# Kernel optimization log

Measured on AMD Instinct MI355X. Metric: run time of the kernel, lower is better.

## Reference

```python
import jax, jax.numpy as jnp
import numpy as np

B, D, H, A, P = 262144, 256, 4, 32, 4
GAMMA = 2.0
SCALE = A ** -0.5
EPS = 1e-5


def _ln(x, g, b):
    m = jnp.mean(x, axis=-1, keepdims=True)
    v = jnp.mean((x - m) ** 2, axis=-1, keepdims=True)
    return (x - m) * jax.lax.rsqrt(v + EPS) * g + b


def setup_inputs() -> dict:
    key = jax.random.key(0)
    ks = jax.random.split(key, 16)
    r = D // 4  # ClassConditionalGate reduction
    return {
        "x": jax.random.normal(ks[0], (B, D), jnp.float32),
        "minority_prob": jax.random.uniform(ks[1], (B, 1), jnp.float32),
        "Wq": jax.random.normal(ks[2], (H, D, A), jnp.float32) * (D ** -0.5),
        "bq": jnp.zeros((H, A), jnp.float32),
        "proto_keys": jax.random.normal(ks[3], (H, P, A), jnp.float32) * 0.02,
        "proto_values": jax.random.normal(ks[4], (H, P, A), jnp.float32) * 0.02,
        "proto_importance": jnp.full((H, P), 1.0 / P, jnp.float32),
        "focal_alpha": jnp.array([0.6 * (1 + 0.1 * i) for i in range(H)], jnp.float32),
        "focal_temp": jnp.ones((H,), jnp.float32),
        "Wo": jax.random.normal(ks[5], (H, A, A), jnp.float32) * (A ** -0.5),
        "bo": jnp.zeros((H, A), jnp.float32),
        "ln_g": jnp.ones((H, A), jnp.float32),
        "ln_b": jnp.zeros((H, A), jnp.float32),
        "Wf": jax.random.normal(ks[6], (H * A, D), jnp.float32) * ((H * A) ** -0.5),
        "bf": jnp.zeros((D,), jnp.float32),
        "Wg1": jax.random.normal(ks[7], (D + 1, r), jnp.float32) * ((D + 1) ** -0.5),
        "bg1": jnp.zeros((r,), jnp.float32),
        "Wg2": jax.random.normal(ks[8], (r, D), jnp.float32) * (r ** -0.5),
        "bg2": jnp.zeros((D,), jnp.float32),
        "lnF_g": jnp.ones((D,), jnp.float32),
        "lnF_b": jnp.zeros((D,), jnp.float32),
    }


def reference(x, minority_prob, Wq, bq, proto_keys, proto_values, proto_importance,
              focal_alpha, focal_temp, Wo, bo, ln_g, ln_b, Wf, bf,
              Wg1, bg1, Wg2, bg2, lnF_g, lnF_b):
    # all heads batched over leading H axis (dropout is identity in eval)
    q = jnp.einsum("bd,hda->bha", x, Wq) + bq                       # [B,H,A]
    scores = jnp.einsum("bha,hpa->bhp", q, proto_keys) + proto_importance
    # focal modulation: uncertainty per sample, per-head alpha/temp
    uncertainty = 1.0 - jnp.abs(minority_prob - 0.5) * 2.0           # [B,1]
    fw = focal_alpha * (uncertainty + 1e-8) ** GAMMA * focal_temp    # [B,H]
    scores = scores * (1.0 + fw[:, :, None])
    w = jax.nn.softmax(scores * SCALE, axis=-1)                      # [B,H,P]
    attended = jnp.einsum("bhp,hpa->bha", w, proto_values)
    h_out = jnp.einsum("bha,hao->bho", attended, Wo) + bo
    h_out = _ln(h_out, ln_g, ln_b)                                   # per-head LN
    combined = h_out.reshape(h_out.shape[0], H * A)                  # cat over heads
    out = combined @ Wf + bf                                         # [B,D]
    # class-conditional gate
    difficulty = 1.0 - 2.0 * jnp.abs(minority_prob - 0.5)            # [B,1]
    gi = jnp.concatenate([out, difficulty], axis=-1)
    gate = jax.nn.sigmoid(jax.nn.relu(gi @ Wg1 + bg1) @ Wg2 + bg2)
    out = out * gate
    return _ln(out + x, lnF_g, lnF_b)
```

## Files before the change

kernel.cpp:

```cpp
#include <hip/hip_runtime.h>
#include <math.h>

typedef __bf16 bf16;
typedef __bf16 bf16x8 __attribute__((ext_vector_type(8)));
typedef float f32x4 __attribute__((ext_vector_type(4)));

#define MFMA16(a,b,c) __builtin_amdgcn_mfma_f32_16x16x32_bf16((a),(b),(c),0,0,0)

#define D 256
#define H 4
#define A 32
#define P 4
#define HA 128
#define RHID 64
#define ROWS 64
#define NROWS_TOT 262144
#define SQP 136
#define SCALE_F 0.17677669529663687f

#define OFF_Q  0
#define OFF_F  32768
#define OFF_G1 65536
#define OFF_G2 81920
#define OFF_O  98304
#define NPACK  102400

__global__ __launch_bounds__(256)
void prep_kernel(const float* __restrict__ Wq, const float* __restrict__ Wf,
                 const float* __restrict__ Wg1, const float* __restrict__ Wg2,
                 const float* __restrict__ Wo, bf16* __restrict__ ws)
{
  int i = blockIdx.x * 256 + threadIdx.x;
  if (i >= NPACK) return;
  float v;
  if (i < OFF_F) {
    int j = i & 7, l = (i >> 3) & 63, nt = (i >> 9) & 1, ks = (i >> 10) & 7, h = i >> 13;
    int k = ks * 32 + (l >> 4) * 8 + j, n = nt * 16 + (l & 15);
    v = Wq[(h * 256 + k) * 32 + n];
  } else if (i < OFF_G1) {
    int ii = i - OFF_F;
    int j = ii & 7, l = (ii >> 3) & 63, g = (ii >> 9) & 15, ks = ii >> 13;
    int k = ks * 32 + (l >> 4) * 8 + j, n = g * 16 + (l & 15);
    v = Wf[k * 256 + n];
  } else if (i < OFF_G2) {
    int ii = i - OFF_G1;
    int j = ii & 7, l = (ii >> 3) & 63, nt = (ii >> 9) & 3, ks = ii >> 11;
    int k = ks * 32 + (l >> 4) * 8 + j, n = nt * 16 + (l & 15);
    v = Wg1[k * 64 + n];
  } else if (i < OFF_O) {
    int ii = i - OFF_G2;
    int j = ii & 7, l = (ii >> 3) & 63, g = (ii >> 9) & 15, ks = ii >> 13;
    int k = ks * 32 + (l >> 4) * 8 + j, n = g * 16 + (l & 15);
    v = Wg2[k * 256 + n];
  } else {
    int ii = i - OFF_O;
    int j = ii & 7, l = (ii >> 3) & 63, nt = (ii >> 9) & 1, h = ii >> 10;
    int k = (l >> 4) * 8 + j, n = nt * 16 + (l & 15);
    v = Wo[(h * 32 + k) * 32 + n];
  }
  ws[i] = (bf16)v;
}

__global__ __launch_bounds__(256, 2)
void faiia_kernel(const float* __restrict__ x, const float* __restrict__ mp,
    const float* __restrict__ bq, const float* __restrict__ pk,
    const float* __restrict__ pv, const float* __restrict__ imp,
    const float* __restrict__ fa, const float* __restrict__ ft,
    const float* __restrict__ bo, const float* __restrict__ lng,
    const float* __restrict__ lnb, const float* __restrict__ bfb,
    const float* __restrict__ Wg1, const float* __restrict__ bg1,
    const float* __restrict__ bg2, const float* __restrict__ lnFg,
    const float* __restrict__ lnFb, const bf16* __restrict__ ws,
    float* __restrict__ out)
{
  __shared__ __attribute__((aligned(16))) bf16 s_regA[16384];
  __shared__ __attribute__((aligned(16))) bf16 s_q[ROWS * SQP];
  __shared__ __attribute__((aligned(16))) bf16 s_hfrag[4096];
  __shared__ float s_pk[H*P*A], s_pv[H*P*A], s_imp[H*P], s_fa[H], s_ft[H];
  __shared__ float s_bq[HA], s_bo[HA], s_lng[HA], s_lnb[HA];
  __shared__ float s_bf[D], s_bg1[RHID], s_wg1d[RHID], s_bg2[D], s_lnFg[D], s_lnFb[D];
  __shared__ float s_diff[ROWS];
  __shared__ float s_lnsum[ROWS*4], s_lnsq[ROWS*4], s_rmean[ROWS], s_rrstd[ROWS];

  const int t = threadIdx.x;
  const int lane = t & 63;
  const int w = t >> 6;
  const int lr = lane >> 4;
  const int lc = lane & 15;
  const int row0 = blockIdx.x * ROWS;

  for (int i = t; i < H*P*A; i += 256) { s_pk[i] = pk[i]; s_pv[i] = pv[i]; }
  if (t < H*P) s_imp[t] = imp[t];
  if (t < H) { s_fa[t] = fa[t]; s_ft[t] = ft[t]; }
  if (t < HA) { s_bq[t] = bq[t]; s_bo[t] = bo[t]; s_lng[t] = lng[t]; s_lnb[t] = lnb[t]; }
  s_bf[t] = bfb[t]; s_bg2[t] = bg2[t]; s_lnFg[t] = lnFg[t]; s_lnFb[t] = lnFb[t];
  if (t < RHID) { s_bg1[t] = bg1[t]; s_wg1d[t] = Wg1[256*RHID + t]; }
  if (t < ROWS) { float m = mp[row0 + t]; s_diff[t] = 1.f - 2.f*fabsf(m - 0.5f); }

  {
    const float* xbase = x + (size_t)row0 * D;
    #pragma unroll
    for (int i = 0; i < 8; ++i) {
      int s = t + 256*i;
      int l = s & 63, ks = (s >> 6) & 7, mt = s >> 9;
      int row = mt*16 + (l & 15);
      int k0 = ks*32 + ((l >> 4) & 3)*8;
      const float* xp = xbase + row*D + k0;
      float4 v0 = *reinterpret_cast<const float4*>(xp);
      float4 v1 = *reinterpret_cast<const float4*>(xp + 4);
      bf16x8 fr;
      fr[0]=(bf16)v0.x; fr[1]=(bf16)v0.y; fr[2]=(bf16)v0.z; fr[3]=(bf16)v0.w;
      fr[4]=(bf16)v1.x; fr[5]=(bf16)v1.y; fr[6]=(bf16)v1.z; fr[7]=(bf16)v1.w;
      *reinterpret_cast<bf16x8*>(&s_regA[(size_t)s * 8]) = fr;
    }
  }
  __syncthreads();

  {
    f32x4 acc[4][2];
    #pragma unroll
    for (int mt = 0; mt < 4; ++mt) { acc[mt][0] = (f32x4)0.f; acc[mt][1] = (f32x4)0.f; }
    const bf16x8* pQ = reinterpret_cast<const bf16x8*>(ws + OFF_Q);
    #pragma unroll
    for (int ks = 0; ks < 8; ++ks) {
      bf16x8 b0 = pQ[((w*8 + ks)*2 + 0)*64 + lane];
      bf16x8 b1 = pQ[((w*8 + ks)*2 + 1)*64 + lane];
      #pragma unroll
      for (int mt = 0; mt < 4; ++mt) {
        bf16x8 a = *reinterpret_cast<const bf16x8*>(&s_regA[((mt*8 + ks)*64 + lane)*8]);
        acc[mt][0] = MFMA16(a, b0, acc[mt][0]);
        acc[mt][1] = MFMA16(a, b1, acc[mt][1]);
      }
    }
    float bq0 = s_bq[w*32 + lc], bq1 = s_bq[w*32 + 16 + lc];
    #pragma unroll
    for (int mt = 0; mt < 4; ++mt)
      #pragma unroll
      for (int r = 0; r < 4; ++r) {
        int row = mt*16 + lr*4 + r;
        s_q[row*SQP + w*32 + lc]      = (bf16)(acc[mt][0][r] + bq0);
        s_q[row*SQP + w*32 + 16 + lc] = (bf16)(acc[mt][1][r] + bq1);
      }
  }
  __syncthreads();

  {
    const int r = t >> 2, h = t & 3;
    float q[32];
    #pragma unroll
    for (int g = 0; g < 4; ++g) {
      bf16x8 v = *reinterpret_cast<const bf16x8*>(&s_q[r*SQP + h*32 + g*8]);
      #pragma unroll
      for (int j = 0; j < 8; ++j) q[g*8 + j] = (float)v[j];
    }
    float u = s_diff[r];
    float up = u + 1e-8f;
    float mod = 1.f + s_fa[h]*up*up*s_ft[h];
    float sc[4];
    #pragma unroll
    for (int p = 0; p < 4; ++p) {
      float s = s_imp[h*4 + p];
      const float4* kp = reinterpret_cast<const float4*>(&s_pk[(h*4 + p)*32]);
      #pragma unroll
      for (int g = 0; g < 8; ++g) {
        float4 kv = kp[g];
        s = fmaf(q[g*4+0], kv.x, s); s = fmaf(q[g*4+1], kv.y, s);
        s = fmaf(q[g*4+2], kv.z, s); s = fmaf(q[g*4+3], kv.w, s);
      }
      sc[p] = s * mod * SCALE_F;
    }
    float mx = fmaxf(fmaxf(sc[0], sc[1]), fmaxf(sc[2], sc[3]));
    float e0 = expf(sc[0]-mx), e1 = expf(sc[1]-mx), e2 = expf(sc[2]-mx), e3 = expf(sc[3]-mx);
    float inv = 1.f / (e0+e1+e2+e3);
    e0 *= inv; e1 *= inv; e2 *= inv; e3 *= inv;
    const float4* p0 = reinterpret_cast<const float4*>(&s_pv[(h*4+0)*32]);
    const float4* p1 = reinterpret_cast<const float4*>(&s_pv[(h*4+1)*32]);
    const float4* p2 = reinterpret_cast<const float4*>(&s_pv[(h*4+2)*32]);
    const float4* p3 = reinterpret_cast<const float4*>(&s_pv[(h*4+3)*32]);
    const int mt = r >> 4, rl = r & 15;
    #pragma unroll
    for (int g = 0; g < 4; ++g) {
      float4 a0 = p0[g*2],   b0v = p0[g*2+1];
      float4 a1 = p1[g*2],   b1v = p1[g*2+1];
      float4 a2 = p2[g*2],   b2v = p2[g*2+1];
      float4 a3 = p3[g*2],   b3v = p3[g*2+1];
      bf16x8 av;
      av[0] = (bf16)(e0*a0.x + e1*a1.x + e2*a2.x + e3*a3.x);
      av[1] = (bf16)(e0*a0.y + e1*a1.y + e2*a2.y + e3*a3.y);
      av[2] = (bf16)(e0*a0.z + e1*a1.z + e2*a2.z + e3*a3.z);
      av[3] = (bf16)(e0*a0.w + e1*a1.w + e2*a2.w + e3*a3.w);
      av[4] = (bf16)(e0*b0v.x + e1*b1v.x + e2*b2v.x + e3*b3v.x);
      av[5] = (bf16)(e0*b0v.y + e1*b1v.y + e2*b2v.y + e3*b3v.y);
      av[6] = (bf16)(e0*b0v.z + e1*b1v.z + e2*b2v.z + e3*b3v.z);
      av[7] = (bf16)(e0*b0v.w + e1*b1v.w + e2*b2v.w + e3*b3v.w);
      *reinterpret_cast<bf16x8*>(&s_regA[(((h*4) + mt)*64 + g*16 + rl)*8]) = av;
    }
  }
  __syncthreads();

  {
    f32x4 acc[4][2];
    #pragma unroll
    for (int mt = 0; mt < 4; ++mt) { acc[mt][0] = (f32x4)0.f; acc[mt][1] = (f32x4)0.f; }
    const bf16x8* pO = reinterpret_cast<const bf16x8*>(ws + OFF_O);
    bf16x8 b0 = pO[(w*2 + 0)*64 + lane];
    bf16x8 b1 = pO[(w*2 + 1)*64 + lane];
    #pragma unroll
    for (int mt = 0; mt < 4; ++mt) {
      bf16x8 a = *reinterpret_cast<const bf16x8*>(&s_regA[((w*4 + mt)*64 + lane)*8]);
      acc[mt][0] = MFMA16(a, b0, acc[mt][0]);
      acc[mt][1] = MFMA16(a, b1, acc[mt][1]);
    }
    float bo0 = s_bo[w*32 + lc],  bo1 = s_bo[w*32 + 16 + lc];
    float lg0 = s_lng[w*32 + lc], lg1 = s_lng[w*32 + 16 + lc];
    float lb0 = s_lnb[w*32 + lc], lb1 = s_lnb[w*32 + 16 + lc];
    #pragma unroll
    for (int mt = 0; mt < 4; ++mt)
      #pragma unroll
      for (int r = 0; r < 4; ++r) {
        float v0 = acc[mt][0][r] + bo0;
        float v1 = acc[mt][1][r] + bo1;
        float s = v0 + v1, sq = v0*v0 + v1*v1;
        s += __shfl_xor(s, 1, 64);  sq += __shfl_xor(sq, 1, 64);
        s += __shfl_xor(s, 2, 64);  sq += __shfl_xor(sq, 2, 64);
        s += __shfl_xor(s, 4, 64);  sq += __shfl_xor(sq, 4, 64);
        s += __shfl_xor(s, 8, 64);  sq += __shfl_xor(sq, 8, 64);
        float mean = s * (1.f/32.f);
        float var  = sq * (1.f/32.f) - mean*mean;
        float rstd = rsqrtf(var + 1e-5f);
        float n0 = (v0 - mean)*rstd*lg0 + lb0;
        float n1 = (v1 - mean)*rstd*lg1 + lb1;
        int rl = lr*4 + r;
        int base = 8192 + ((w*4 + mt)*64)*8;
        s_regA[base + (16*(lc >> 3)       + rl)*8 + (lane & 7)] = (bf16)n0;
        s_regA[base + (16*(2 + (lc >> 3)) + rl)*8 + (lane & 7)] = (bf16)n1;
      }
  }
  __syncthreads();

  f32x4 acc2[4][4];
  {
    #pragma unroll
    for (int mt = 0; mt < 4; ++mt)
      #pragma unroll
      for (int nt = 0; nt < 4; ++nt) acc2[mt][nt] = (f32x4)0.f;
    const bf16x8* pF = reinterpret_cast<const bf16x8*>(ws + OFF_F);
    #pragma unroll
    for (int ks = 0; ks < 4; ++ks) {
      bf16x8 a[4], bb[4];
      #pragma unroll
      for (int mt = 0; mt < 4; ++mt)
        a[mt] = *reinterpret_cast<const bf16x8*>(&s_regA[8192 + ((ks*4 + mt)*64 + lane)*8]);
      #pragma unroll
      for (int nt = 0; nt < 4; ++nt)
        bb[nt] = pF[(ks*16 + w*4 + nt)*64 + lane];
      #pragma unroll
      for (int mt = 0; mt < 4; ++mt)
        #pragma unroll
        for (int nt = 0; nt < 4; ++nt)
          acc2[mt][nt] = MFMA16(a[mt], bb[nt], acc2[mt][nt]);
    }
    #pragma unroll
    for (int nt = 0; nt < 4; ++nt) {
      float bfv = s_bf[w*64 + nt*16 + lc];
      #pragma unroll
      for (int mt = 0; mt < 4; ++mt)
        #pragma unroll
        for (int r = 0; r < 4; ++r) acc2[mt][nt][r] += bfv;
    }
  }
  __syncthreads();
  {
    #pragma unroll
    for (int mt = 0; mt < 4; ++mt)
      #pragma unroll
      for (int nt = 0; nt < 4; ++nt) {
        int ks3 = w*2 + (nt >> 1);
        #pragma unroll
        for (int r = 0; r < 4; ++r) {
          int lane2 = 16*((nt & 1)*2 + (lc >> 3)) + (lr*4 + r);
          s_regA[((ks3*4 + mt)*64 + lane2)*8 + (lane & 7)] = (bf16)acc2[mt][nt][r];
        }
      }
  }
  __syncthreads();

  {
    f32x4 acc3[4];
    #pragma unroll
    for (int mt = 0; mt < 4; ++mt) acc3[mt] = (f32x4)0.f;
    const bf16x8* pG1 = reinterpret_cast<const bf16x8*>(ws + OFF_G1);
    #pragma unroll
    for (int ks = 0; ks < 8; ++ks) {
      bf16x8 b = pG1[(ks*4 + w)*64 + lane];
      #pragma unroll
      for (int mt = 0; mt < 4; ++mt) {
        bf16x8 a = *reinterpret_cast<const bf16x8*>(&s_regA[((ks*4 + mt)*64 + lane)*8]);
        acc3[mt] = MFMA16(a, b, acc3[mt]);
      }
    }
    int col3 = w*16 + lc;
    float b1v = s_bg1[col3], wdv = s_wg1d[col3];
    #pragma unroll
    for (int mt = 0; mt < 4; ++mt)
      #pragma unroll
      for (int r = 0; r < 4; ++r) {
        int row = mt*16 + lr*4 + r;
        float hv = acc3[mt][r] + b1v + s_diff[row]*wdv;
        hv = fmaxf(hv, 0.f);
        s_hfrag[(((w >> 1)*4 + mt)*64 + 16*((w & 1)*2 + (lc >> 3)) + (lr*4 + r))*8 + (lane & 7)] = (bf16)hv;
      }
  }
  __syncthreads();

  {
    f32x4 acc4[4][4];
    #pragma unroll
    for (int mt = 0; mt < 4; ++mt)
      #pragma unroll
      for (int nt = 0; nt < 4; ++nt) acc4[mt][nt] = (f32x4)0.f;
    const bf16x8* pG2 = reinterpret_cast<const bf16x8*>(ws + OFF_G2);
    #pragma unroll
    for (int ks = 0; ks < 2; ++ks) {
      bf16x8 a[4], bb[4];
      #pragma unroll
      for (int mt = 0; mt < 4; ++mt)
        a[mt] = *reinterpret_cast<const bf16x8*>(&s_hfrag[((ks*4 + mt)*64 + lane)*8]);
      #pragma unroll
      for (int nt = 0; nt < 4; ++nt)
        bb[nt] = pG2[(ks*16 + w*4 + nt)*64 + lane];
      #pragma unroll
      for (int mt = 0; mt < 4; ++mt)
        #pragma unroll
        for (int nt = 0; nt < 4; ++nt)
          acc4[mt][nt] = MFMA16(a[mt], bb[nt], acc4[mt][nt]);
    }
    const float* xbase = x + (size_t)row0 * D;
    #pragma unroll
    for (int nt = 0; nt < 4; ++nt) {
      int c = w*64 + nt*16 + lc;
      float bg2v = s_bg2[c];
      #pragma unroll
      for (int mt = 0; mt < 4; ++mt)
        #pragma unroll
        for (int r = 0; r < 4; ++r) {
          int row = mt*16 + lr*4 + r;
          float gate = 1.f / (1.f + expf(-(acc4[mt][nt][r] + bg2v)));
          acc2[mt][nt][r] = acc2[mt][nt][r]*gate + xbase[row*D + c];
        }
    }
  }
  {
    #pragma unroll
    for (int mt = 0; mt < 4; ++mt)
      #pragma unroll
      for (int r = 0; r < 4; ++r) {
        float s = 0.f, sq = 0.f;
        #pragma unroll
        for (int nt = 0; nt < 4; ++nt) {
          float v = acc2[mt][nt][r];
          s += v; sq = fmaf(v, v, sq);
        }
        s += __shfl_xor(s, 1, 64);  sq += __shfl_xor(sq, 1, 64);
        s += __shfl_xor(s, 2, 64);  sq += __shfl_xor(sq, 2, 64);
        s += __shfl_xor(s, 4, 64);  sq += __shfl_xor(sq, 4, 64);
        s += __shfl_xor(s, 8, 64);  sq += __shfl_xor(sq, 8, 64);
        if (lc == 0) {
          int row = mt*16 + lr*4 + r;
          s_lnsum[row*4 + w] = s;
          s_lnsq[row*4 + w]  = sq;
        }
      }
  }
  __syncthreads();
  if (t < ROWS) {
    float s  = s_lnsum[t*4] + s_lnsum[t*4+1] + s_lnsum[t*4+2] + s_lnsum[t*4+3];
    float sq = s_lnsq[t*4]  + s_lnsq[t*4+1]  + s_lnsq[t*4+2]  + s_lnsq[t*4+3];
    float mean = s * (1.f/256.f);
    float var  = sq * (1.f/256.f) - mean*mean;
    s_rmean[t] = mean;
    s_rrstd[t] = rsqrtf(var + 1e-5f);
  }
  __syncthreads();
  {
    float* obase = out + (size_t)row0 * D;
    #pragma unroll
    for (int mt = 0; mt < 4; ++mt)
      #pragma unroll
      for (int r = 0; r < 4; ++r) {
        int row = mt*16 + lr*4 + r;
        float mean = s_rmean[row], rstd = s_rrstd[row];
        #pragma unroll
        for (int nt = 0; nt < 4; ++nt) {
          int c = w*64 + nt*16 + lc;
          obase[row*D + c] = (acc2[mt][nt][r] - mean)*rstd*s_lnFg[c] + s_lnFb[c];
        }
      }
  }
}

extern "C" void kernel_launch(void* const* d_in, const int* in_sizes, int n_in,
                              void* d_out, int out_size, void* d_ws, size_t ws_size,
                              hipStream_t stream) {
  (void)in_sizes; (void)n_in; (void)ws_size; (void)out_size;
  const float* x   = (const float*)d_in[0];
  const float* mp  = (const float*)d_in[1];
  const float* Wq  = (const float*)d_in[2];
  const float* bq  = (const float*)d_in[3];
  const float* pk  = (const float*)d_in[4];
  const float* pv  = (const float*)d_in[5];
  const float* imp = (const float*)d_in[6];
  const float* fa  = (const float*)d_in[7];
  const float* ft  = (const float*)d_in[8];
  const float* Wo  = (const float*)d_in[9];
  const float* bo  = (const float*)d_in[10];
  const float* lng = (const float*)d_in[11];
  const float* lnb = (const float*)d_in[12];
  const float* Wf  = (const float*)d_in[13];
  const float* bf  = (const float*)d_in[14];
  const float* Wg1 = (const float*)d_in[15];
  const float* bg1 = (const float*)d_in[16];
  const float* Wg2 = (const float*)d_in[17];
  const float* bg2 = (const float*)d_in[18];
  const float* lnFg= (const float*)d_in[19];
  const float* lnFb= (const float*)d_in[20];
  float* out = (float*)d_out;
  bf16* ws = (bf16*)d_ws;

  hipLaunchKernelGGL(prep_kernel, dim3((NPACK + 255)/256), dim3(256), 0, stream,
                     Wq, Wf, Wg1, Wg2, Wo, ws);
  hipLaunchKernelGGL(faiia_kernel, dim3(NROWS_TOT / ROWS), dim3(256), 0, stream,
                     x, mp, bq, pk, pv, imp, fa, ft, bo, lng, lnb,
                     bf, Wg1, bg1, bg2, lnFg, lnFb, ws, out);
}
```

Before: 262.6 us.

## Alias shared buffers to cut LDS, raise occupancy, use fast exp/rcp

Removes the dedicated padded s_q and LN-stat shared arrays by aliasing them onto the upper half of s_regA and onto s_hfrag. An XOR swizzle on s_q replaces the padding to avoid bank conflicts, and extra barriers guard the aliased reuse. Launch bounds go from 2 to 3 blocks per CU so more blocks can be resident. Softmax and the sigmoid gate now use __expf and a hardware reciprocal, which trades a little accuracy for fewer instructions, while the extra barriers and tighter register budget add cost.

```diff
diff --git a/kernel.cpp b/kernel.cpp
--- a/kernel.cpp
+++ b/kernel.cpp
@@ -15,7 +15,6 @@
 #define RHID 64
 #define ROWS 64
 #define NROWS_TOT 262144
-#define SQP 136
 #define SCALE_F 0.17677669529663687f
 
 #define OFF_Q  0
@@ -24,6 +23,9 @@
 #define OFF_G2 81920
 #define OFF_O  98304
 #define NPACK  102400
+
+__device__ __forceinline__ float fast_exp(float x) { return __expf(x); }
+__device__ __forceinline__ float fast_rcp(float x) { return __builtin_amdgcn_rcpf(x); }
 
 __global__ __launch_bounds__(256)
 void prep_kernel(const float* __restrict__ Wq, const float* __restrict__ Wf,
@@ -61,7 +63,7 @@
   ws[i] = (bf16)v;
 }
 
-__global__ __launch_bounds__(256, 2)
+__global__ __launch_bounds__(256, 3)
 void faiia_kernel(const float* __restrict__ x, const float* __restrict__ mp,
     const float* __restrict__ bq, const float* __restrict__ pk,
     const float* __restrict__ pv, const float* __restrict__ imp,
@@ -74,13 +76,17 @@
     float* __restrict__ out)
 {
   __shared__ __attribute__((aligned(16))) bf16 s_regA[16384];
-  __shared__ __attribute__((aligned(16))) bf16 s_q[ROWS * SQP];
   __shared__ __attribute__((aligned(16))) bf16 s_hfrag[4096];
   __shared__ float s_pk[H*P*A], s_pv[H*P*A], s_imp[H*P], s_fa[H], s_ft[H];
   __shared__ float s_bq[HA], s_bo[HA], s_lng[HA], s_lnb[HA];
   __shared__ float s_bf[D], s_bg1[RHID], s_wg1d[RHID], s_bg2[D], s_lnFg[D], s_lnFb[D];
   __shared__ float s_diff[ROWS];
-  __shared__ float s_lnsum[ROWS*4], s_lnsq[ROWS*4], s_rmean[ROWS], s_rrstd[ROWS];
+
+  bf16* s_q = s_regA + 8192;
+  float* s_lnsum = reinterpret_cast<float*>(s_hfrag);
+  float* s_lnsq  = s_lnsum + 256;
+  float* s_rmean = s_lnsq + 256;
+  float* s_rrstd = s_rmean + 64;
 
   const int t = threadIdx.x;
   const int lane = t & 63;
@@ -132,24 +138,30 @@
         acc[mt][1] = MFMA16(a, b1, acc[mt][1]);
       }
     }
+    __syncthreads();
     float bq0 = s_bq[w*32 + lc], bq1 = s_bq[w*32 + 16 + lc];
     #pragma unroll
     for (int mt = 0; mt < 4; ++mt)
       #pragma unroll
       for (int r = 0; r < 4; ++r) {
         int row = mt*16 + lr*4 + r;
-        s_q[row*SQP + w*32 + lc]      = (bf16)(acc[mt][0][r] + bq0);
-        s_q[row*SQP + w*32 + 16 + lc] = (bf16)(acc[mt][1][r] + bq1);
+        int sw = (row & 7) << 3;
+        int c0 = (w*32 + lc) ^ sw;
+        int c1 = (w*32 + 16 + lc) ^ sw;
+        s_q[row*128 + c0] = (bf16)(acc[mt][0][r] + bq0);
+        s_q[row*128 + c1] = (bf16)(acc[mt][1][r] + bq1);
       }
   }
   __syncthreads();
 
   {
     const int r = t >> 2, h = t & 3;
+    const int swr = (r & 7) << 3;
     float q[32];
     #pragma unroll
     for (int g = 0; g < 4; ++g) {
-      bf16x8 v = *reinterpret_cast<const bf16x8*>(&s_q[r*SQP + h*32 + g*8]);
+      int c0 = (h*32 + g*8) ^ swr;
+      bf16x8 v = *reinterpret_cast<const bf16x8*>(&s_q[r*128 + c0]);
       #pragma unroll
       for (int j = 0; j < 8; ++j) q[g*8 + j] = (float)v[j];
     }
@@ -170,8 +182,9 @@
       sc[p] = s * mod * SCALE_F;
     }
     float mx = fmaxf(fmaxf(sc[0], sc[1]), fmaxf(sc[2], sc[3]));
-    float e0 = expf(sc[0]-mx), e1 = expf(sc[1]-mx), e2 = expf(sc[2]-mx), e3 = expf(sc[3]-mx);
-    float inv = 1.f / (e0+e1+e2+e3);
+    float e0 = fast_exp(sc[0]-mx), e1 = fast_exp(sc[1]-mx);
+    float e2 = fast_exp(sc[2]-mx), e3 = fast_exp(sc[3]-mx);
+    float inv = fast_rcp(e0+e1+e2+e3);
     e0 *= inv; e1 *= inv; e2 *= inv; e3 *= inv;
     const float4* p0 = reinterpret_cast<const float4*>(&s_pv[(h*4+0)*32]);
     const float4* p1 = reinterpret_cast<const float4*>(&s_pv[(h*4+1)*32]);
@@ -335,6 +348,7 @@
         for (int nt = 0; nt < 4; ++nt)
           acc4[mt][nt] = MFMA16(a[mt], bb[nt], acc4[mt][nt]);
     }
+    __syncthreads();
     const float* xbase = x + (size_t)row0 * D;
     #pragma unroll
     for (int nt = 0; nt < 4; ++nt) {
@@ -345,7 +359,8 @@
         #pragma unroll
         for (int r = 0; r < 4; ++r) {
           int row = mt*16 + lr*4 + r;
-          float gate = 1.f / (1.f + expf(-(acc4[mt][nt][r] + bg2v)));
+          float z = acc4[mt][nt][r] + bg2v;
+          float gate = fast_rcp(1.f + fast_exp(-z));
           acc2[mt][nt][r] = acc2[mt][nt][r]*gate + xbase[row*D + c];
         }
     }
```

Measured after the change: 374.8 us. +42.7%, slower.
